# Performance work log

Hardware: AMD Instinct MI355X
Metric: run time of the kernel (lower is better)

## Reference

```python
import jax, jax.numpy as jnp
import numpy as np
import math

KSIZE = 2.0
SIGMA = 3.0
EPS = 1e-05


def setup_inputs() -> dict:
    key = jax.random.key(0)
    kx, ky, kz = jax.random.split(key, 3)
    N, D = 8192, 64
    X = jax.random.normal(kx, (N, D), dtype=jnp.float32)
    Y = jax.random.normal(ky, (N, D), dtype=jnp.float32)
    Z = jax.random.normal(kz, (N, D), dtype=jnp.float32)
    return {"X": X, "Y": Y, "Z": Z}


def _mean_kernel(A, B, ksize):
    # mean over N x N RBF Gram: exp(-||a-b||^2 / ksize) / sqrt(2*pi*ksize)
    # squared distances via expansion (same math as sum((a-b)**2, -1))
    sq = (jnp.sum(A * A, axis=-1)[:, None]
          + jnp.sum(B * B, axis=-1)[None, :]
          - 2.0 * A @ B.T)
    norm = math.sqrt(2.0 * math.pi * ksize)
    return jnp.mean(jnp.exp(-sq / ksize)) / norm


def reference(X, Y, Z):
    ks = KSIZE
    mxx = _mean_kernel(X, X, ks)
    mzz = _mean_kernel(Z, Z, ks)
    mxz = _mean_kernel(X, Z, ks)
    mxy = _mean_kernel(X, Y, ks)
    myy = _mean_kernel(Y, Y, ks)
    myz = _mean_kernel(Y, Z, ks)
    r1 = jnp.log(SIGMA * jnp.sqrt(mxx * mzz + EPS) / (mxz + EPS))
    r2 = jnp.log(SIGMA * jnp.sqrt(myy * mzz + EPS) / (myz + EPS))
    r3 = jnp.log(SIGMA * jnp.sqrt(mxx * myy + EPS) / (mxy + EPS))
    return r1 * 10.0 + r2 + r3 * 10.0
```

## Files before the change

kernel.cpp:

```cpp
#include <hip/hip_runtime.h>
#include <math.h>

#define N 8192
#define D 64

typedef short bf16x8 __attribute__((ext_vector_type(8)));
typedef float f32x4 __attribute__((ext_vector_type(4)));

__device__ __forceinline__ void gload_lds16(const void* g, void* l) {
    __builtin_amdgcn_global_load_lds(
        (const __attribute__((address_space(1))) void*)g,
        (__attribute__((address_space(3))) void*)l, 16, 0, 0);
}

__global__ void init_accs(float* accs) {
    if (threadIdx.x < 6) accs[threadIdx.x] = 0.0f;
}

__global__ __launch_bounds__(256) void convert_norm(
        const float* __restrict__ X, const float* __restrict__ Y,
        const float* __restrict__ Z,
        unsigned short* __restrict__ bmat, float* __restrict__ nscl) {
    int wid  = blockIdx.x * 4 + (threadIdx.x >> 6);
    int lane = threadIdx.x & 63;
    int mat  = wid >> 13;
    int row  = wid & 8191;
    const float* src = (mat == 0) ? X : (mat == 1 ? Y : Z);
    float v = src[row * D + lane] * 1.2011224087864498f;
    unsigned int bits = __builtin_bit_cast(unsigned int, v);
    unsigned short us = (unsigned short)((bits + 0x7FFFu + ((bits >> 16) & 1u)) >> 16);
    float f = __builtin_bit_cast(float, (unsigned int)us << 16);
    bmat[(size_t)mat * (N * D) + row * D + lane] = us;
    float sq = f * f;
    #pragma unroll
    for (int off = 32; off; off >>= 1) sq += __shfl_xor(sq, off);
    if (lane == 0) nscl[mat * N + row] = sq * 0.5f;
}

__global__ __launch_bounds__(256, 6) void gram_kernel(
        const unsigned short* __restrict__ bmat,
        const float* __restrict__ nscl,
        float* __restrict__ accs) {
    const int PA[6] = {0, 2, 0, 0, 1, 1};
    const int PB[6] = {0, 2, 2, 1, 1, 2};
    int p  = blockIdx.y;
    int bx = blockIdx.x;
    int ti = bx >> 1;
    int tc = bx & 1;

    const unsigned short* A = bmat + (size_t)PA[p] * (N * D);
    const unsigned short* B = bmat + (size_t)PB[p] * (N * D);
    const float* ca = nscl + PA[p] * N;
    const float* cb = nscl + PB[p] * N;

    int tid = threadIdx.x;
    int w = tid >> 6, lane = tid & 63;
    int wr = w >> 1, wc = w & 1;
    int rowBase = ti * 64 + wr * 32;
    int r = lane & 15, q = lane >> 4, r7 = lane & 7;

    __shared__ __align__(128) char lds[3 * 8192];
    __shared__ float wsum[4];

    int sub = w * 2048;
    int laneoff = ((lane >> 3) << 7) + ((r7 ^ (lane >> 3)) << 4);
    const char* gB = (const char*)(B + (size_t)(tc * 4096) * D);

    int off0 = wc * 4096 + r * 128 + ((q ^ r7) << 4);
    int off1 = wc * 4096 + r * 128 + (((4 + q) ^ r7) << 4);

    {
        const char* g0 = gB + sub + laneoff;
        gload_lds16(g0,        lds + sub);
        gload_lds16(g0 + 1024, lds + sub + 1024);
        const char* g1 = gB + 8192 + sub + laneoff;
        gload_lds16(g1,        lds + 8192 + sub);
        gload_lds16(g1 + 1024, lds + 8192 + sub + 1024);
    }

    bf16x8 afrag[2][2];
    #pragma unroll
    for (int mt = 0; mt < 2; ++mt)
        #pragma unroll
        for (int kc = 0; kc < 2; ++kc)
            afrag[mt][kc] = *reinterpret_cast<const bf16x8*>(
                A + (size_t)(rowBase + mt * 16 + r) * D + kc * 32 + q * 8);
    f32x4 ncam[2];
    #pragma unroll
    for (int mt = 0; mt < 2; ++mt)
        #pragma unroll
        for (int e = 0; e < 4; ++e)
            ncam[mt][e] = -ca[rowBase + mt * 16 + q * 4 + e];

    const float* cbp = cb + tc * 4096 + wc * 32 + r;

    f32x4 lsum = (f32x4)0.0f;
    unsigned rb = 0;

    for (int t = 0; t < 64; ++t) {
        asm volatile("s_waitcnt vmcnt(2)" ::: "memory");
        __builtin_amdgcn_s_barrier();
        asm volatile("" ::: "memory");

        float cb0 = cbp[0], cb1 = cbp[16];

        unsigned sb = rb + 16384; if (sb >= 24576) sb -= 24576;
        int tn = (t + 2 <= 63) ? (t + 2) : 63;
        const char* gs = gB + (size_t)tn * 8192 + sub + laneoff;
        gload_lds16(gs,        lds + sb + sub);
        gload_lds16(gs + 1024, lds + sb + sub + 1024);

        const char* lb = lds + rb;
        bf16x8 bfrag[2][2];
        bfrag[0][0] = *reinterpret_cast<const bf16x8*>(lb + off0);
        bfrag[0][1] = *reinterpret_cast<const bf16x8*>(lb + off1);
        bfrag[1][0] = *reinterpret_cast<const bf16x8*>(lb + 2048 + off0);
        bfrag[1][1] = *reinterpret_cast<const bf16x8*>(lb + 2048 + off1);

        f32x4 acc[2][2];
        acc[0][0] = ncam[0] - cb0; acc[0][1] = ncam[0] - cb1;
        acc[1][0] = ncam[1] - cb0; acc[1][1] = ncam[1] - cb1;

        #pragma unroll
        for (int kc = 0; kc < 2; ++kc)
            #pragma unroll
            for (int mt = 0; mt < 2; ++mt)
                #pragma unroll
                for (int nt = 0; nt < 2; ++nt)
                    acc[mt][nt] = __builtin_amdgcn_mfma_f32_16x16x32_bf16(
                        afrag[mt][kc], bfrag[nt][kc], acc[mt][nt], 0, 0, 0);

        f32x4 vm = acc[0][0];
        #pragma unroll
        for (int mt = 0; mt < 2; ++mt)
            #pragma unroll
            for (int nt = 0; nt < 2; ++nt)
                if (mt | nt)
                    #pragma unroll
                    for (int e = 0; e < 4; ++e)
                        vm[e] = fmaxf(vm[e], acc[mt][nt][e]);
        float m = fmaxf(fmaxf(vm[0], vm[1]), fmaxf(vm[2], vm[3]));

        if (__any(m > -30.0f)) {
            #pragma unroll
            for (int mt = 0; mt < 2; ++mt) {
                #pragma unroll
                for (int nt = 0; nt < 2; ++nt) {
                    f32x4 ex;
                    #pragma unroll
                    for (int e = 0; e < 4; ++e)
                        ex[e] = __builtin_amdgcn_exp2f(acc[mt][nt][e]);
                    lsum += ex;
                }
            }
        }

        cbp += 64;
        rb += 8192; if (rb >= 24576) rb = 0;
    }

    float ls = lsum[0] + lsum[1] + lsum[2] + lsum[3];
    #pragma unroll
    for (int off = 32; off; off >>= 1) ls += __shfl_xor(ls, off);
    if (lane == 0) wsum[w] = ls;
    __syncthreads();
    if (tid == 0)
        atomicAdd(&accs[p], wsum[0] + wsum[1] + wsum[2] + wsum[3]);
}

__global__ void finalize_kernel(const float* __restrict__ accs,
                                float* __restrict__ out) {
    double inv = 1.0 / (8192.0 * 8192.0 * 3.5449077018110318);
    double mxx = accs[0] * inv, mzz = accs[1] * inv, mxz = accs[2] * inv;
    double mxy = accs[3] * inv, myy = accs[4] * inv, myz = accs[5] * inv;
    double r1 = log(3.0 * sqrt(mxx * mzz + 1e-5) / (mxz + 1e-5));
    double r2 = log(3.0 * sqrt(myy * mzz + 1e-5) / (myz + 1e-5));
    double r3 = log(3.0 * sqrt(mxx * myy + 1e-5) / (mxy + 1e-5));
    out[0] = (float)(10.0 * r1 + r2 + 10.0 * r3);
}

extern "C" void kernel_launch(void* const* d_in, const int* in_sizes, int n_in,
                              void* d_out, int out_size, void* d_ws, size_t ws_size,
                              hipStream_t stream) {
    const float* X = (const float*)d_in[0];
    const float* Y = (const float*)d_in[1];
    const float* Z = (const float*)d_in[2];
    char* ws = (char*)d_ws;
    unsigned short* bmat = (unsigned short*)ws;
    float* nscl = (float*)(ws + (size_t)3 * N * D * 2);
    float* accs = (float*)(ws + (size_t)3 * N * D * 2 + (size_t)3 * N * 4);
    float* out = (float*)d_out;

    hipLaunchKernelGGL(init_accs, dim3(1), dim3(64), 0, stream, accs);
    hipLaunchKernelGGL(convert_norm, dim3(3 * N / 4), dim3(256), 0, stream,
                       X, Y, Z, bmat, nscl);
    hipLaunchKernelGGL(gram_kernel, dim3(256, 6), dim3(256), 0, stream,
                       bmat, nscl, accs);
    hipLaunchKernelGGL(finalize_kernel, dim3(1), dim3(1), 0, stream, accs, out);
}
```

Before: 83.09 us.

## Software-pipeline gram loop so exp epilogue overlaps next tile's MFMAs

Unrolls the 64-step tile loop by three, with fixed LDS ring offsets so the buffer-index arithmetic goes away. The max-check and exp2 epilogue for the previous tile's accumulators now runs after the current tile's LDS fragment loads are issued and before its MFMAs, so transcendental work can overlap matrix-core latency. It also flattens the max reduction into a balanced tree. The cost is three accumulator sets live at once, which raises register pressure and may hurt occupancy.

After: 79.48 us. 4.4% less time.

```diff
diff --git a/kernel.cpp b/kernel.cpp
--- a/kernel.cpp
+++ b/kernel.cpp
@@ -95,69 +95,72 @@
     const float* cbp = cb + tc * 4096 + wc * 32 + r;
 
     f32x4 lsum = (f32x4)0.0f;
-    unsigned rb = 0;
-
-    for (int t = 0; t < 64; ++t) {
-        asm volatile("s_waitcnt vmcnt(2)" ::: "memory");
-        __builtin_amdgcn_s_barrier();
-        asm volatile("" ::: "memory");
-
-        float cb0 = cbp[0], cb1 = cbp[16];
-
-        unsigned sb = rb + 16384; if (sb >= 24576) sb -= 24576;
-        int tn = (t + 2 <= 63) ? (t + 2) : 63;
-        const char* gs = gB + (size_t)tn * 8192 + sub + laneoff;
-        gload_lds16(gs,        lds + sb + sub);
-        gload_lds16(gs + 1024, lds + sb + sub + 1024);
-
-        const char* lb = lds + rb;
-        bf16x8 bfrag[2][2];
-        bfrag[0][0] = *reinterpret_cast<const bf16x8*>(lb + off0);
-        bfrag[0][1] = *reinterpret_cast<const bf16x8*>(lb + off1);
-        bfrag[1][0] = *reinterpret_cast<const bf16x8*>(lb + 2048 + off0);
-        bfrag[1][1] = *reinterpret_cast<const bf16x8*>(lb + 2048 + off1);
-
-        f32x4 acc[2][2];
-        acc[0][0] = ncam[0] - cb0; acc[0][1] = ncam[0] - cb1;
-        acc[1][0] = ncam[1] - cb0; acc[1][1] = ncam[1] - cb1;
-
-        #pragma unroll
-        for (int kc = 0; kc < 2; ++kc)
-            #pragma unroll
-            for (int mt = 0; mt < 2; ++mt)
-                #pragma unroll
-                for (int nt = 0; nt < 2; ++nt)
-                    acc[mt][nt] = __builtin_amdgcn_mfma_f32_16x16x32_bf16(
-                        afrag[mt][kc], bfrag[nt][kc], acc[mt][nt], 0, 0, 0);
-
-        f32x4 vm = acc[0][0];
-        #pragma unroll
-        for (int mt = 0; mt < 2; ++mt)
-            #pragma unroll
-            for (int nt = 0; nt < 2; ++nt)
-                if (mt | nt)
-                    #pragma unroll
-                    for (int e = 0; e < 4; ++e)
-                        vm[e] = fmaxf(vm[e], acc[mt][nt][e]);
-        float m = fmaxf(fmaxf(vm[0], vm[1]), fmaxf(vm[2], vm[3]));
-
-        if (__any(m > -30.0f)) {
-            #pragma unroll
-            for (int mt = 0; mt < 2; ++mt) {
-                #pragma unroll
-                for (int nt = 0; nt < 2; ++nt) {
-                    f32x4 ex;
-                    #pragma unroll
-                    for (int e = 0; e < 4; ++e)
-                        ex[e] = __builtin_amdgcn_exp2f(acc[mt][nt][e]);
-                    lsum += ex;
-                }
-            }
-        }
-
-        cbp += 64;
-        rb += 8192; if (rb >= 24576) rb = 0;
-    }
+    f32x4 acc0[2][2], acc1[2][2], acc2[2][2];
+
+    #define EPI(ACC)                                                          \
+    {                                                                         \
+        float e0 = fmaxf(fmaxf(ACC[0][0][0], ACC[0][0][1]), ACC[0][0][2]);    \
+        float e1 = fmaxf(fmaxf(ACC[0][0][3], ACC[0][1][0]), ACC[0][1][1]);    \
+        float e2 = fmaxf(fmaxf(ACC[0][1][2], ACC[0][1][3]), ACC[1][0][0]);    \
+        float e3 = fmaxf(fmaxf(ACC[1][0][1], ACC[1][0][2]), ACC[1][0][3]);    \
+        float e4 = fmaxf(fmaxf(ACC[1][1][0], ACC[1][1][1]), ACC[1][1][2]);    \
+        float e5 = fmaxf(fmaxf(e0, e1), e2);                                  \
+        float e6 = fmaxf(fmaxf(e3, e4), ACC[1][1][3]);                        \
+        float em = fmaxf(e5, e6);                                             \
+        if (__any(em > -30.0f)) {                                             \
+            _Pragma("unroll")                                                 \
+            for (int mt = 0; mt < 2; ++mt) {                                  \
+                _Pragma("unroll")                                             \
+                for (int nt = 0; nt < 2; ++nt) {                              \
+                    f32x4 ex;                                                 \
+                    _Pragma("unroll")                                         \
+                    for (int e = 0; e < 4; ++e)                               \
+                        ex[e] = __builtin_amdgcn_exp2f(ACC[mt][nt][e]);       \
+                    lsum += ex;                                               \
+                }                                                             \
+            }                                                                 \
+        }                                                                     \
+    }
+
+    #define GSTEP(RB, SB, ACC, DO_EPI, ACCP, TT)                              \
+    {                                                                         \
+        asm volatile("s_waitcnt vmcnt(2)" ::: "memory");                      \
+        __builtin_amdgcn_s_barrier();                                         \
+        asm volatile("" ::: "memory");                                        \
+        float cb0 = cbp[0], cb1 = cbp[16];                                    \
+        int tn = ((TT) + 2 <= 63) ? ((TT) + 2) : 63;                          \
+        const char* gs = gB + (size_t)tn * 8192 + sub + laneoff;              \
+        gload_lds16(gs,        lds + (SB) + sub);                             \
+        gload_lds16(gs + 1024, lds + (SB) + sub + 1024);                      \
+        bf16x8 bf00 = *reinterpret_cast<const bf16x8*>(lds + (RB) + off0);    \
+        bf16x8 bf01 = *reinterpret_cast<const bf16x8*>(lds + (RB) + off1);    \
+        bf16x8 bf10 = *reinterpret_cast<const bf16x8*>(lds + (RB) + 2048 + off0); \
+        bf16x8 bf11 = *reinterpret_cast<const bf16x8*>(lds + (RB) + 2048 + off1); \
+        if (DO_EPI) EPI(ACCP);                                                \
+        ACC[0][0] = ncam[0] - cb0; ACC[0][1] = ncam[0] - cb1;                 \
+        ACC[1][0] = ncam[1] - cb0; ACC[1][1] = ncam[1] - cb1;                 \
+        ACC[0][0] = __builtin_amdgcn_mfma_f32_16x16x32_bf16(afrag[0][0], bf00, ACC[0][0], 0, 0, 0); \
+        ACC[0][1] = __builtin_amdgcn_mfma_f32_16x16x32_bf16(afrag[0][0], bf10, ACC[0][1], 0, 0, 0); \
+        ACC[1][0] = __builtin_amdgcn_mfma_f32_16x16x32_bf16(afrag[1][0], bf00, ACC[1][0], 0, 0, 0); \
+        ACC[1][1] = __builtin_amdgcn_mfma_f32_16x16x32_bf16(afrag[1][0], bf10, ACC[1][1], 0, 0, 0); \
+        ACC[0][0] = __builtin_amdgcn_mfma_f32_16x16x32_bf16(afrag[0][1], bf01, ACC[0][0], 0, 0, 0); \
+        ACC[0][1] = __builtin_amdgcn_mfma_f32_16x16x32_bf16(afrag[0][1], bf11, ACC[0][1], 0, 0, 0); \
+        ACC[1][0] = __builtin_amdgcn_mfma_f32_16x16x32_bf16(afrag[1][1], bf01, ACC[1][0], 0, 0, 0); \
+        ACC[1][1] = __builtin_amdgcn_mfma_f32_16x16x32_bf16(afrag[1][1], bf11, ACC[1][1], 0, 0, 0); \
+        cbp += 64;                                                            \
+    }
+
+    GSTEP(0, 16384, acc0, false, acc0, 0)
+    for (int trip = 0; trip < 21; ++trip) {
+        int t1 = 1 + trip * 3;
+        GSTEP(8192,  0,     acc1, true, acc0, t1)
+        GSTEP(16384, 8192,  acc2, true, acc1, t1 + 1)
+        GSTEP(0,     16384, acc0, true, acc2, t1 + 2)
+    }
+    EPI(acc0)
+
+    #undef GSTEP
+    #undef EPI
 
     float ls = lsum[0] + lsum[1] + lsum[2] + lsum[3];
     #pragma unroll
```
